# Kernel optimization log

Hardware: AMD Instinct MI355X
Metric: run time of the kernel (lower is better)

The kernel has to match this reference:

```python
import jax, jax.numpy as jnp
import numpy as np

N_NODES = 50000
NUM_REL = 8
IN_DIM = 128
HID = 256
NUM_CLASSES = 2
E = 1600000
M = 200000
LN_EPS = 1e-5


def setup_inputs() -> dict:
    key = jax.random.key(0)
    ks = jax.random.split(key, 20)
    s = 0.05
    inp = {
        "x": jax.random.normal(ks[0], (N_NODES, IN_DIM), jnp.float32),
        "edge_index": jax.random.randint(ks[1], (2, E), 0, N_NODES, jnp.int32),
        "edge_type": jax.random.randint(ks[2], (E,), 0, NUM_REL, jnp.int32),
        "dec_edges": jax.random.randint(ks[3], (M, 2), 0, N_NODES, jnp.int32),
        # conv1
        "W1": jax.random.normal(ks[4], (NUM_REL, IN_DIM, HID), jnp.float32) * s,
        "root1": jax.random.normal(ks[5], (IN_DIM, HID), jnp.float32) * s,
        "b1": jnp.zeros((HID,), jnp.float32),
        # conv2
        "W2": jax.random.normal(ks[6], (NUM_REL, HID, HID), jnp.float32) * s,
        "root2": jax.random.normal(ks[7], (HID, HID), jnp.float32) * s,
        "b2": jnp.zeros((HID,), jnp.float32),
        # layernorms
        "ln1_g": jnp.ones((HID,), jnp.float32),
        "ln1_b": jnp.zeros((HID,), jnp.float32),
        "ln2_g": jnp.ones((HID,), jnp.float32),
        "ln2_b": jnp.zeros((HID,), jnp.float32),
        # edge MLP: 2*HID -> HID -> HID//2 -> NUM_CLASSES
        "mlp_w1": jax.random.normal(ks[8], (2 * HID, HID), jnp.float32) * s,
        "mlp_b1": jnp.zeros((HID,), jnp.float32),
        "mlp_w2": jax.random.normal(ks[9], (HID, HID // 2), jnp.float32) * s,
        "mlp_b2": jnp.zeros((HID // 2,), jnp.float32),
        "mlp_w3": jax.random.normal(ks[10], (HID // 2, NUM_CLASSES), jnp.float32) * s,
        "mlp_b3": jnp.zeros((NUM_CLASSES,), jnp.float32),
    }
    return inp


def layer_norm(h, g, b):
    mu = jnp.mean(h, axis=-1, keepdims=True)
    var = jnp.mean(jnp.square(h - mu), axis=-1, keepdims=True)
    return (h - mu) * jax.lax.rsqrt(var + LN_EPS) * g + b


def rgcn_conv(x, edge_index, edge_type, W, root, bias):
    # PyG RGCNConv with aggr='mean': per-relation mean aggregation of
    # neighbor features, aggregate-then-transform (valid since linear),
    # plus root transform and bias.
    src, dst = edge_index[0], edge_index[1]
    xs = x[src]  # [E, d_in]
    out = x @ root + bias
    num_rel = W.shape[0]
    for r in range(num_rel):
        m = (edge_type == r).astype(x.dtype)  # [E]
        agg = jax.ops.segment_sum(xs * m[:, None], dst, num_segments=x.shape[0])
        cnt = jax.ops.segment_sum(m, dst, num_segments=x.shape[0])
        out = out + (agg / jnp.maximum(cnt, 1.0)[:, None]) @ W[r]
    return out


def reference(x, edge_index, edge_type, dec_edges,
              W1, root1, b1, W2, root2, b2,
              ln1_g, ln1_b, ln2_g, ln2_b,
              mlp_w1, mlp_b1, mlp_w2, mlp_b2, mlp_w3, mlp_b3):
    # encode (dropout is identity in eval mode)
    h1 = rgcn_conv(x, edge_index, edge_type, W1, root1, b1)
    h1 = layer_norm(jax.nn.relu(h1), ln1_g, ln1_b)
    h2 = rgcn_conv(h1, edge_index, edge_type, W2, root2, b2)
    h2 = layer_norm(jax.nn.relu(h2), ln2_g, ln2_b)
    h = h1 + h2
    # decode: gather endpoints, concat, MLP (exact-erf GELU as nn.GELU)
    z = jnp.concatenate([h[dec_edges[:, 0]], h[dec_edges[:, 1]]], axis=1)
    z = jax.nn.gelu(z @ mlp_w1 + mlp_b1, approximate=False)
    z = jax.nn.gelu(z @ mlp_w2 + mlp_b2, approximate=False)
    return z @ mlp_w3 + mlp_b3
```

## Files before the change

### kernel.cpp

```cpp
#include <hip/hip_runtime.h>
#include <math.h>

typedef __attribute__((ext_vector_type(8))) short short8;
typedef __attribute__((ext_vector_type(4))) float f32x4;
typedef __attribute__((address_space(3))) void lds_void;
typedef const __attribute__((address_space(1))) void glb_void;

#define N_NODES 50000
#define NUM_REL 8
#define IN_DIM 128
#define HID 256
#define E_EDGES 1600000
#define M_DEC 200000
#define K1 1152
#define K2 2304
#define LN_EPS 1e-5f
#define NBUCK ((N_NODES + 63) >> 6)
#define NSEG (N_NODES * 8)
#define NSEG_BLK ((NSEG + 1023) >> 10)

__device__ __forceinline__ float b2f(ushort u) {
    union { unsigned int i; float f; } v; v.i = ((unsigned int)u) << 16; return v.f;
}
__device__ __forceinline__ ushort f2b(float f) {
    union { float f; unsigned int i; } v; v.f = f;
    unsigned int r = v.i + 0x7FFFu + ((v.i >> 16) & 1u);
    return (ushort)(r >> 16);
}
__device__ __forceinline__ unsigned int pk2(ushort a, ushort b) {
    return (unsigned int)a | ((unsigned int)b << 16);
}
__device__ __forceinline__ float gelu_fast(float x) {
    float y = 1.5957691216f * (x + 0.044715f * x * x * x);
    float e = __expf(y);
    float t = 1.f - 2.f * __builtin_amdgcn_rcpf(e + 1.f);
    return 0.5f * x * (1.f + t);
}

__global__ void count_all(const int* __restrict__ ei, const int* __restrict__ et,
                          int* __restrict__ cnt2,
                          const int* __restrict__ dec, int* __restrict__ bcnt) {
    int e = blockIdx.x * 256 + threadIdx.x;
    if (e < E_EDGES) {
        int dst = ei[E_EDGES + e];
        int r = et[e] & 7;
        atomicAdd(&cnt2[dst * 8 + r], 1);
    }
    if (e < M_DEC) {
        int a = dec[(size_t)e * 2];
        if (a < 0) a = 0; if (a >= N_NODES) a = N_NODES - 1;
        atomicAdd(&bcnt[a >> 6], 1);
    }
}

__global__ __launch_bounds__(1024) void scan_pass1(const int* __restrict__ cnt,
                                                   int* __restrict__ outp,
                                                   int* __restrict__ bsum) {
    __shared__ int ts[1024];
    const int t = threadIdx.x;
    const int i = blockIdx.x * 1024 + t;
    int v = (i < NSEG) ? cnt[i] : 0;
    ts[t] = v;
    __syncthreads();
#pragma unroll
    for (int off = 1; off < 1024; off <<= 1) {
        int u = (t >= off) ? ts[t - off] : 0;
        __syncthreads();
        ts[t] += u;
        __syncthreads();
    }
    if (i < NSEG) outp[i] = ts[t] - v;
    if (t == 1023) bsum[blockIdx.x] = ts[1023];
}

__global__ __launch_bounds__(1024) void scan_mid(int* __restrict__ bsum, int* __restrict__ rp2,
                                                 const int* __restrict__ bcnt,
                                                 int* __restrict__ bptr) {
    __shared__ int ts[1024];
    const int t = threadIdx.x;
    if (blockIdx.x == 0) {
        int v = (t < NSEG_BLK) ? bsum[t] : 0;
        ts[t] = v;
        __syncthreads();
#pragma unroll
        for (int off = 1; off < 1024; off <<= 1) {
            int u = (t >= off) ? ts[t - off] : 0;
            __syncthreads();
            ts[t] += u;
            __syncthreads();
        }
        if (t < NSEG_BLK) bsum[t] = ts[t] - v;
        if (t == NSEG_BLK - 1) rp2[NSEG] = ts[t];
    } else {
        int v = (t < NBUCK) ? bcnt[t] : 0;
        ts[t] = v;
        __syncthreads();
#pragma unroll
        for (int off = 1; off < 1024; off <<= 1) {
            int u = (t >= off) ? ts[t - off] : 0;
            __syncthreads();
            ts[t] += u;
            __syncthreads();
        }
        if (t < NBUCK) bptr[t] = ts[t] - v;
        if (t == 1023) bptr[NBUCK] = ts[1023];
    }
}

__global__ __launch_bounds__(1024) void scan_pass3(int* __restrict__ outp,
                                                   const int* __restrict__ bsum) {
    const int i = blockIdx.x * 1024 + threadIdx.x;
    if (i < NSEG) outp[i] += bsum[blockIdx.x];
}

__global__ void fill_all(const int* __restrict__ ei, const int* __restrict__ et,
                         const int* __restrict__ rp2, int* __restrict__ cursor,
                         unsigned int* __restrict__ epk,
                         const int* __restrict__ dec, const int* __restrict__ bptr,
                         int* __restrict__ bcur, int* __restrict__ perm) {
    int e = blockIdx.x * 256 + threadIdx.x;
    if (e < E_EDGES) {
        int src = ei[e];
        int dst = ei[E_EDGES + e];
        int r   = et[e] & 7;
        int idx8 = dst * 8 + r;
        int pos = rp2[idx8] + atomicAdd(&cursor[idx8], 1);
        if (pos >= 0 && pos < E_EDGES) epk[pos] = (unsigned int)src;
    }
    if (e < M_DEC) {
        int a = dec[(size_t)e * 2];
        if (a < 0) a = 0; if (a >= N_NODES) a = N_NODES - 1;
        int b = a >> 6;
        int pos = bptr[b] + atomicAdd(&bcur[b], 1);
        if (pos >= 0 && pos < M_DEC) perm[pos] = e;
    }
}

__global__ void pack_all(const float* __restrict__ x, ushort* __restrict__ xb,
                         const float* __restrict__ root1, const float* __restrict__ W1,
                         const float* __restrict__ root2, const float* __restrict__ W2,
                         ushort* __restrict__ B1t, ushort* __restrict__ B2t,
                         const float* __restrict__ mw1, const float* __restrict__ mw2,
                         ushort* __restrict__ wuvt, ushort* __restrict__ w2t) {
    const int XC = N_NODES * IN_DIM / 4;
    const int N1 = HID * K1;
    const int N2 = HID * K2;
    const int NU = 512 * 256;
    const int NW = 128 * 256;
    int idx = blockIdx.x * 256 + threadIdx.x;
    if (idx < XC) {
        float4 v = *(const float4*)(x + (size_t)idx * 4);
        uint2 o;
        o.x = pk2(f2b(v.x), f2b(v.y));
        o.y = pk2(f2b(v.z), f2b(v.w));
        *(uint2*)(xb + (size_t)idx * 4) = o;
        return;
    }
    idx -= XC;
    if (idx < N1) {
        int n = idx / K1, k = idx % K1;
        float v;
        if (k < IN_DIM) v = root1[k * HID + n];
        else { int kk = k - IN_DIM; v = W1[(size_t)(kk >> 7) * IN_DIM * HID + (kk & 127) * HID + n]; }
        B1t[(size_t)n * K1 + k] = f2b(v);
        return;
    }
    idx -= N1;
    if (idx < N2) {
        int n = idx / K2, k = idx % K2;
        float v;
        if (k < HID) v = root2[k * HID + n];
        else { int kk = k - HID; v = W2[(size_t)(kk >> 8) * HID * HID + (kk & 255) * HID + n]; }
        B2t[(size_t)n * K2 + k] = f2b(v);
        return;
    }
    idx -= N2;
    if (idx < NU) {
        int n = idx / 256, k = idx % 256;
        float v = (n < 256) ? mw1[(size_t)k * 256 + n] : mw1[(size_t)(256 + k) * 256 + (n - 256)];
        wuvt[(size_t)n * 256 + k] = f2b(v);
        return;
    }
    idx -= NU;
    if (idx < NW) {
        int n = idx / 256, k = idx % 256;
        w2t[n * 256 + k] = f2b(mw2[k * 128 + n]);
    }
}


#define FL1() { int c_ = segend - segbeg; float inv_ = c_ > 0 ? 1.f / (float)c_ : 0.f; \
    *(unsigned int*)(Arow + IN_DIM + r * IN_DIM + 2 * lane) = \
        pk2(f2b((aA.x + aB.x) * inv_), f2b((aA.y + aB.y) * inv_)); \
    aA.x = 0.f; aA.y = 0.f; aB.x = 0.f; aB.y = 0.f; \
    ++r; segbeg = segend; segend = (r < 8) ? rp[r + 1] : end; \
    if (segend < segbeg) segend = segbeg; if (segend > end) segend = end; }
#define CK1(EI) { while (r < 8 && (EI) >= segend) FL1(); }
#define AC1A(U) { aA.x += b2f((ushort)((U) & 0xFFFFu)); aA.y += b2f((ushort)((U) >> 16)); }
#define AC1B(U) { aB.x += b2f((ushort)((U) & 0xFFFFu)); aB.y += b2f((ushort)((U) >> 16)); }

__global__ __launch_bounds__(256) void agg1_kernel(const ushort* __restrict__ xb,
                                                   const int* __restrict__ rp2,
                                                   const unsigned int* __restrict__ epk,
                                                   ushort* __restrict__ Achunk, int n0, int m) {
    const int w = threadIdx.x >> 6, lane = threadIdx.x & 63;
    const int local = blockIdx.x * 4 + w;
    if (local >= m) return;
    const int n = n0 + local;
    const int* rp = rp2 + n * 8;
    ushort* Arow = Achunk + (size_t)local * K1;
    const ushort* xbb = xb + 2 * lane;
    *(unsigned int*)(Arow + 2 * lane) = *(const unsigned int*)(xb + (size_t)n * IN_DIM + 2 * lane);

    int beg = rp[0], end = rp[8];
    if (beg < 0) beg = 0;
    if (end > E_EDGES) end = E_EDGES;
    if (end < beg) end = beg;

    float2 aA = {0.f, 0.f}, aB = {0.f, 0.f};
    int r = 0, segbeg = beg, segend = rp[1];
    if (segend < segbeg) segend = segbeg; if (segend > end) segend = end;

    int e = beg;
    for (; e + 7 < end; e += 8) {
        unsigned int p0 = epk[e],     p1 = epk[e + 1], p2 = epk[e + 2], p3 = epk[e + 3];
        unsigned int p4 = epk[e + 4], p5 = epk[e + 5], p6 = epk[e + 6], p7 = epk[e + 7];
        unsigned int u0 = *(const unsigned int*)(xbb + (size_t)p0 * IN_DIM);
        unsigned int u1 = *(const unsigned int*)(xbb + (size_t)p1 * IN_DIM);
        unsigned int u2 = *(const unsigned int*)(xbb + (size_t)p2 * IN_DIM);
        unsigned int u3 = *(const unsigned int*)(xbb + (size_t)p3 * IN_DIM);
        unsigned int u4 = *(const unsigned int*)(xbb + (size_t)p4 * IN_DIM);
        unsigned int u5 = *(const unsigned int*)(xbb + (size_t)p5 * IN_DIM);
        unsigned int u6 = *(const unsigned int*)(xbb + (size_t)p6 * IN_DIM);
        unsigned int u7 = *(const unsigned int*)(xbb + (size_t)p7 * IN_DIM);
        CK1(e)     AC1A(u0) CK1(e + 1) AC1B(u1)
        CK1(e + 2) AC1A(u2) CK1(e + 3) AC1B(u3)
        CK1(e + 4) AC1A(u4) CK1(e + 5) AC1B(u5)
        CK1(e + 6) AC1A(u6) CK1(e + 7) AC1B(u7)
    }
    for (; e < end; ++e) {
        unsigned int p = epk[e];
        unsigned int u = *(const unsigned int*)(xbb + (size_t)p * IN_DIM);
        CK1(e) AC1A(u)
    }
    while (r < 8) FL1();
}

#define FL2() { int c_ = segend - segbeg; float inv_ = c_ > 0 ? 1.f / (float)c_ : 0.f; \
    f32x4 t_ = aA + aB; uint2 o_; \
    o_.x = pk2(f2b(t_[0] * inv_), f2b(t_[1] * inv_)); \
    o_.y = pk2(f2b(t_[2] * inv_), f2b(t_[3] * inv_)); \
    *(uint2*)(Arow + HID + r * HID + 4 * lane) = o_; \
    aA = (f32x4){0.f, 0.f, 0.f, 0.f}; aB = aA; \
    ++r; segbeg = segend; segend = (r < 8) ? rp[r + 1] : end; \
    if (segend < segbeg) segend = segbeg; if (segend > end) segend = end; }
#define CK2(EI) { while (r < 8 && (EI) >= segend) FL2(); }
#define AC2A(U) { f32x4 f_; \
    f_[0] = b2f((ushort)((U).x & 0xFFFFu)); f_[1] = b2f((ushort)((U).x >> 16)); \
    f_[2] = b2f((ushort)((U).y & 0xFFFFu)); f_[3] = b2f((ushort)((U).y >> 16)); aA += f_; }
#define AC2B(U) { f32x4 f_; \
    f_[0] = b2f((ushort)((U).x & 0xFFFFu)); f_[1] = b2f((ushort)((U).x >> 16)); \
    f_[2] = b2f((ushort)((U).y & 0xFFFFu)); f_[3] = b2f((ushort)((U).y >> 16)); aB += f_; }

__global__ __launch_bounds__(256) void agg2_kernel(const ushort* __restrict__ h1,
                                                   const int* __restrict__ rp2,
                                                   const unsigned int* __restrict__ epk,
                                                   ushort* __restrict__ Achunk, int n0, int m) {
    const int w = threadIdx.x >> 6, lane = threadIdx.x & 63;
    const int local = blockIdx.x * 4 + w;
    if (local >= m) return;
    const int n = n0 + local;
    const int* rp = rp2 + n * 8;
    ushort* Arow = Achunk + (size_t)local * K2;
    const ushort* hb = h1 + 4 * lane;
    *(uint2*)(Arow + 4 * lane) = *(const uint2*)(h1 + (size_t)n * HID + 4 * lane);

    int beg = rp[0], end = rp[8];
    if (beg < 0) beg = 0;
    if (end > E_EDGES) end = E_EDGES;
    if (end < beg) end = beg;

    f32x4 aA = {0.f, 0.f, 0.f, 0.f}, aB = {0.f, 0.f, 0.f, 0.f};
    int r = 0, segbeg = beg, segend = rp[1];
    if (segend < segbeg) segend = segbeg; if (segend > end) segend = end;

    int e = beg;
    for (; e + 7 < end; e += 8) {
        unsigned int p0 = epk[e],     p1 = epk[e + 1], p2 = epk[e + 2], p3 = epk[e + 3];
        unsigned int p4 = epk[e + 4], p5 = epk[e + 5], p6 = epk[e + 6], p7 = epk[e + 7];
        uint2 u0 = *(const uint2*)(hb + (size_t)p0 * HID);
        uint2 u1 = *(const uint2*)(hb + (size_t)p1 * HID);
        uint2 u2 = *(const uint2*)(hb + (size_t)p2 * HID);
        uint2 u3 = *(const uint2*)(hb + (size_t)p3 * HID);
        uint2 u4 = *(const uint2*)(hb + (size_t)p4 * HID);
        uint2 u5 = *(const uint2*)(hb + (size_t)p5 * HID);
        uint2 u6 = *(const uint2*)(hb + (size_t)p6 * HID);
        uint2 u7 = *(const uint2*)(hb + (size_t)p7 * HID);
        CK2(e)     AC2A(u0) CK2(e + 1) AC2B(u1)
        CK2(e + 2) AC2A(u2) CK2(e + 3) AC2B(u3)
        CK2(e + 4) AC2A(u4) CK2(e + 5) AC2B(u5)
        CK2(e + 6) AC2A(u6) CK2(e + 7) AC2B(u7)
    }
    for (; e < end; ++e) {
        unsigned int p = epk[e];
        uint2 u = *(const uint2*)(hb + (size_t)p * HID);
        CK2(e) AC2A(u)
    }
    while (r < 8) FL2();
}


#define STAGE(BUF, KO) { \
    __builtin_amdgcn_global_load_lds((glb_void*)(Ab + (KO)), \
        (lds_void*)(AsBase + (BUF) * 4096 + wave * 8 * 64), 16, 0, 0); \
    _Pragma("unroll") \
    for (int j_ = 0; j_ < 4; ++j_) \
        __builtin_amdgcn_global_load_lds((glb_void*)(Bb + (size_t)j_ * 8 * K + (KO)), \
            (lds_void*)(BsBase + (BUF) * 16384 + (wave * 32 + j_ * 8) * 64), 16, 0, 0); }

#define COMPUTE(CUR) { \
    _Pragma("unroll") \
    for (int kk = 0; kk < 2; ++kk) { \
        const int gsw = (((kk * 4 + qd) ^ (cc & 7)) * 8); \
        short8 af[2], bfv[4]; \
        _Pragma("unroll") \
        for (int i = 0; i < 2; ++i) \
            af[i] = *(const short8*)&AsBase[(CUR) * 4096 + (mh * 32 + i * 16 + cc) * 64 + gsw]; \
        _Pragma("unroll") \
        for (int j = 0; j < 4; ++j) \
            bfv[j] = *(const short8*)&BsBase[(CUR) * 16384 + (wn + j * 16 + cc) * 64 + gsw]; \
        _Pragma("unroll") \
        for (int i = 0; i < 2; ++i) \
            _Pragma("unroll") \
            for (int j = 0; j < 4; ++j) \
                acc[i][j] = __builtin_amdgcn_mfma_f32_16x16x32_bf16(af[i], bfv[j], acc[i][j], 0, 0, 0); \
    } }

__global__ __launch_bounds__(512, 4) void gemm_fused(
    const ushort* __restrict__ A, const ushort* __restrict__ Bt,
    int lda, int M, int K,
    const float* __restrict__ bias, const float* __restrict__ g,
    const float* __restrict__ bvec, const ushort* __restrict__ resid,
    ushort* __restrict__ outp, int ldc, int rowOff) {
    __shared__ __align__(16) ushort smem[40960];
    ushort* AsBase = smem;
    ushort* BsBase = smem + 2 * 64 * 64;
    const int tid = threadIdx.x;
    const int wave = tid >> 6, lane = tid & 63;
    const int w4 = wave & 3, mh = wave >> 2;
    const int cc = lane & 15, qd = lane >> 4;
    const int row0 = blockIdx.x * 64;
    const int colBase = blockIdx.y * 256;
    const int wn = w4 * 64;
    const int srow = lane >> 3;
    const int sgrp = (lane & 7) ^ (srow & 7);
    f32x4 acc[2][4];
#pragma unroll
    for (int i = 0; i < 2; ++i)
#pragma unroll
        for (int j = 0; j < 4; ++j) acc[i][j] = (f32x4){0.f, 0.f, 0.f, 0.f};

    const ushort* Ab = A + (size_t)(row0 + wave * 8 + srow) * lda + sgrp * 8;
    const ushort* Bb = Bt + (size_t)(colBase + wave * 32 + srow) * K + sgrp * 8;

    STAGE(0, 0)
    for (int k0 = 0; k0 < K; k0 += 128) {
        if (k0 + 64 < K) {
            STAGE(1, k0 + 64)
            asm volatile("s_waitcnt vmcnt(5)" ::: "memory");
        } else {
            asm volatile("s_waitcnt vmcnt(0)" ::: "memory");
        }
        __builtin_amdgcn_s_barrier();
        COMPUTE(0)
        asm volatile("s_waitcnt lgkmcnt(0)" ::: "memory");
        __builtin_amdgcn_s_barrier();

        if (k0 + 128 < K) {
            STAGE(0, k0 + 128)
            asm volatile("s_waitcnt vmcnt(5)" ::: "memory");
        } else {
            asm volatile("s_waitcnt vmcnt(0)" ::: "memory");
        }
        __builtin_amdgcn_s_barrier();
        COMPUTE(1)
        asm volatile("s_waitcnt lgkmcnt(0)" ::: "memory");
        __builtin_amdgcn_s_barrier();
    }

    if (g) {
        float* partS = (float*)smem;
        float* partQ = (float*)smem + 256;
        float* muS   = (float*)smem + 512;
        float* rsS   = (float*)smem + 576;
#pragma unroll
        for (int j = 0; j < 4; ++j) {
            float bcol = bias[wn + j * 16 + cc];
#pragma unroll
            for (int i = 0; i < 2; ++i)
#pragma unroll
                for (int r = 0; r < 4; ++r)
                    acc[i][j][r] = fmaxf(acc[i][j][r] + bcol, 0.f);
        }
#pragma unroll
        for (int i = 0; i < 2; ++i)
#pragma unroll
            for (int r = 0; r < 4; ++r) {
                float s = acc[i][0][r] + acc[i][1][r] + acc[i][2][r] + acc[i][3][r];
                float q = acc[i][0][r] * acc[i][0][r] + acc[i][1][r] * acc[i][1][r]
                        + acc[i][2][r] * acc[i][2][r] + acc[i][3][r] * acc[i][3][r];
#pragma unroll
                for (int off = 1; off <= 8; off <<= 1) {
                    s += __shfl_xor(s, off, 64);
                    q += __shfl_xor(q, off, 64);
                }
                if (cc == 0) {
                    int row = mh * 32 + i * 16 + qd * 4 + r;
                    partS[row * 4 + w4] = s;
                    partQ[row * 4 + w4] = q;
                }
            }
        __syncthreads();
        if (tid < 64) {
            float S = partS[tid * 4] + partS[tid * 4 + 1] + partS[tid * 4 + 2] + partS[tid * 4 + 3];
            float Q = partQ[tid * 4] + partQ[tid * 4 + 1] + partQ[tid * 4 + 2] + partQ[tid * 4 + 3];
            float mu = S * (1.f / 256.f);
            float var = Q * (1.f / 256.f) - mu * mu;
            muS[tid] = mu;
            rsS[tid] = rsqrtf(fmaxf(var, 0.f) + LN_EPS);
        }
        __syncthreads();
#pragma unroll
        for (int i = 0; i < 2; ++i)
#pragma unroll
            for (int r = 0; r < 4; ++r) {
                int row = mh * 32 + i * 16 + qd * 4 + r;
                int grow = row0 + row;
                if (grow >= M) continue;
                float mu = muS[row], rs = rsS[row];
                size_t base = (size_t)(rowOff + grow) * ldc;
#pragma unroll
                for (int j = 0; j < 4; ++j) {
                    int col = wn + j * 16 + cc;
                    float val = (acc[i][j][r] - mu) * rs * g[col] + bvec[col];
                    if (resid) val += b2f(resid[base + col]);
                    outp[base + col] = f2b(val);
                }
            }
    } else {
#pragma unroll
        for (int i = 0; i < 2; ++i)
#pragma unroll
            for (int r = 0; r < 4; ++r) {
                int grow = row0 + mh * 32 + i * 16 + qd * 4 + r;
                if (grow >= M) continue;
                size_t base = (size_t)(rowOff + grow) * ldc;
#pragma unroll
                for (int j = 0; j < 4; ++j) {
                    int col = colBase + wn + j * 16 + cc;
                    outp[base + col] = f2b(acc[i][j][r]);
                }
            }
    }
}

__global__ __launch_bounds__(256) void edge_kernel(
    const ushort* __restrict__ uv, const int* __restrict__ dec, const int* __restrict__ perm,
    const float* __restrict__ b1, const ushort* __restrict__ w2t,
    const float* __restrict__ b2, const float* __restrict__ w3,
    const float* __restrict__ b3, float* __restrict__ outp, int M) {
    __shared__ __align__(16) ushort z1s[64][264];
    __shared__ __align__(16) ushort z2s[64][136];
    __shared__ float b1s[256], b2s[128], w3s[256];
    const int tid = threadIdx.x;
    const int wave = tid >> 6, lane = tid & 63;
    const int cc = lane & 15, qd = lane >> 4, lk = qd * 8, rr = qd * 4;
    const int e0 = blockIdx.x * 64;

    b1s[tid] = b1[tid];
    if (tid < 128) b2s[tid] = b2[tid];
    w3s[tid] = w3[tid];
    __syncthreads();

    {
        int e = tid >> 2, seg = tid & 3;
        int ge = perm[e0 + e];
        if (ge < 0) ge = 0; if (ge >= M) ge = M - 1;
        int a = dec[(size_t)ge * 2];
        int b = dec[(size_t)ge * 2 + 1];
        if (a < 0) a = 0; if (a >= N_NODES) a = N_NODES - 1;
        if (b < 0) b = 0; if (b >= N_NODES) b = N_NODES - 1;
        const ushort* up = uv + (size_t)a * 512 + seg * 64;
        const ushort* vp = uv + (size_t)b * 512 + 256 + seg * 64;
        short8 us[8], vs[8];
#pragma unroll
        for (int j = 0; j < 8; ++j) us[j] = *(const short8*)(up + j * 8);
#pragma unroll
        for (int j = 0; j < 8; ++j) vs[j] = *(const short8*)(vp + j * 8);
        int d0 = seg * 64;
#pragma unroll
        for (int j = 0; j < 8; ++j) {
            int d = d0 + j * 8;
            short8 zs;
#pragma unroll
            for (int l = 0; l < 8; ++l) {
                float z = b2f((ushort)us[j][l]) + b2f((ushort)vs[j][l]) + b1s[d + l];
                zs[l] = (short)f2b(gelu_fast(z));
            }
            *(short8*)&z1s[e][d] = zs;
        }
    }
    __syncthreads();

    f32x4 acc[4][2];
#pragma unroll
    for (int i = 0; i < 4; ++i)
#pragma unroll
        for (int j = 0; j < 2; ++j) acc[i][j] = (f32x4){0.f, 0.f, 0.f, 0.f};
    const int n0 = wave * 32;
#pragma unroll
    for (int ks = 0; ks < 8; ++ks) {
        short8 af[4], bfv[2];
#pragma unroll
        for (int i = 0; i < 4; ++i) af[i] = *(const short8*)&z1s[i * 16 + cc][ks * 32 + lk];
#pragma unroll
        for (int j = 0; j < 2; ++j)
            bfv[j] = *(const short8*)(w2t + (size_t)(n0 + j * 16 + cc) * 256 + ks * 32 + lk);
#pragma unroll
        for (int i = 0; i < 4; ++i)
#pragma unroll
            for (int j = 0; j < 2; ++j)
                acc[i][j] = __builtin_amdgcn_mfma_f32_16x16x32_bf16(af[i], bfv[j], acc[i][j], 0, 0, 0);
    }
#pragma unroll
    for (int i = 0; i < 4; ++i)
#pragma unroll
        for (int j = 0; j < 2; ++j)
#pragma unroll
            for (int r = 0; r < 4; ++r) {
                int m = i * 16 + rr + r;
                int n = n0 + j * 16 + cc;
                z2s[m][n] = f2b(gelu_fast(acc[i][j][r] + b2s[n]));
            }
    __syncthreads();

    if (tid < 128) {
        int e = tid >> 1, c = tid & 1;
        float s = b3[c];
        for (int k = 0; k < 128; ++k) s += b2f(z2s[e][k]) * w3s[k * 2 + c];
        int ge = perm[e0 + e];
        if (ge >= 0 && ge < M) outp[(size_t)ge * 2 + c] = s;
    }
}

extern "C" void kernel_launch(void* const* d_in, const int* in_sizes, int n_in,
                              void* d_out, int out_size, void* d_ws, size_t ws_size,
                              hipStream_t stream) {
    const float* x          = (const float*)d_in[0];
    const int*   edge_index = (const int*)d_in[1];
    const int*   edge_type  = (const int*)d_in[2];
    const int*   dec_edges  = (const int*)d_in[3];
    const float* W1         = (const float*)d_in[4];
    const float* root1      = (const float*)d_in[5];
    const float* b1         = (const float*)d_in[6];
    const float* W2         = (const float*)d_in[7];
    const float* root2      = (const float*)d_in[8];
    const float* b2         = (const float*)d_in[9];
    const float* ln1_g      = (const float*)d_in[10];
    const float* ln1_b      = (const float*)d_in[11];
    const float* ln2_g      = (const float*)d_in[12];
    const float* ln2_b      = (const float*)d_in[13];
    const float* mlp_w1     = (const float*)d_in[14];
    const float* mlp_b1     = (const float*)d_in[15];
    const float* mlp_w2     = (const float*)d_in[16];
    const float* mlp_b2     = (const float*)d_in[17];
    const float* mlp_w3     = (const float*)d_in[18];
    const float* mlp_b3     = (const float*)d_in[19];

    char* ws = (char*)d_ws;
    size_t off = 0;
    auto alloc = [&](size_t bytes) {
        void* p = ws + off;
        off += (bytes + 255) & ~(size_t)255;
        return p;
    };
    unsigned int* epk     = (unsigned int*)alloc((size_t)E_EDGES * 4);
    int*          rp2     = (int*)alloc((size_t)(NSEG + 1) * 4);
    int*          tmp     = (int*)alloc((size_t)(NSEG + NBUCK) * 4);
    int*          tmpb    = tmp + NSEG;
    int*          bptr    = (int*)alloc((size_t)(NBUCK + 1) * 4);
    int*          bsum    = (int*)alloc((size_t)NSEG_BLK * 4);
    int*          perm    = (int*)alloc((size_t)M_DEC * 4);
    ushort*       B1t     = (ushort*)alloc((size_t)HID * K1 * 2);
    ushort*       B2t     = (ushort*)alloc((size_t)HID * K2 * 2);
    ushort*       wuvt    = (ushort*)alloc((size_t)512 * 256 * 2);
    ushort*       w2t     = (ushort*)alloc((size_t)128 * 256 * 2);
    ushort*       xb      = (ushort*)alloc((size_t)N_NODES * IN_DIM * 2);
    ushort*       hfin    = (ushort*)alloc((size_t)N_NODES * HID * 2);

    size_t regionOff = off;
    ushort* h1ln  = (ushort*)(ws + regionOff);
    ushort* uvbuf = h1ln;
    size_t h1b = (((size_t)N_NODES * HID * 2) + 255) & ~(size_t)255;
    ushort* Achunk = (ushort*)(ws + regionOff + h1b);
    long long chunkB = (long long)ws_size - (long long)(regionOff + h1b);
    int chunk = 64;
    if (chunkB > 0) {
        long long c = chunkB / ((long long)K2 * 2);
        if (c > N_NODES) c = N_NODES;
        c &= ~63LL;
        if (c >= 64) chunk = (int)c;
    }
    int chunk1 = chunk * 2;
    if (chunk1 > N_NODES) chunk1 = N_NODES;

    hipMemsetAsync(tmp, 0, (size_t)(NSEG + NBUCK) * 4, stream);
    count_all<<<(E_EDGES + 255) / 256, 256, 0, stream>>>(edge_index, edge_type, tmp, dec_edges, tmpb);
    scan_pass1<<<NSEG_BLK, 1024, 0, stream>>>(tmp, rp2, bsum);
    scan_mid<<<2, 1024, 0, stream>>>(bsum, rp2, tmpb, bptr);
    scan_pass3<<<NSEG_BLK, 1024, 0, stream>>>(rp2, bsum);
    hipMemsetAsync(tmp, 0, (size_t)(NSEG + NBUCK) * 4, stream);
    fill_all<<<(E_EDGES + 255) / 256, 256, 0, stream>>>(edge_index, edge_type, rp2, tmp, epk,
                                                        dec_edges, bptr, tmpb, perm);

    {
        int total = N_NODES * IN_DIM / 4 + HID * K1 + HID * K2 + 512 * 256 + 128 * 256;
        pack_all<<<(total + 255) / 256, 256, 0, stream>>>(x, xb, root1, W1, root2, W2,
                                                          B1t, B2t, mlp_w1, mlp_w2, wuvt, w2t);
    }

    for (int n0 = 0; n0 < N_NODES; n0 += chunk1) {
        int m = N_NODES - n0; if (m > chunk1) m = chunk1;
        agg1_kernel<<<(m + 3) / 4, 256, 0, stream>>>(xb, rp2, epk, Achunk, n0, m);
        gemm_fused<<<dim3((m + 63) / 64, 1), 512, 0, stream>>>(
            Achunk, B1t, K1, m, K1, b1, ln1_g, ln1_b, nullptr, h1ln, HID, n0);
    }
    for (int n0 = 0; n0 < N_NODES; n0 += chunk) {
        int m = N_NODES - n0; if (m > chunk) m = chunk;
        agg2_kernel<<<(m + 3) / 4, 256, 0, stream>>>(h1ln, rp2, epk, Achunk, n0, m);
        gemm_fused<<<dim3((m + 63) / 64, 1), 512, 0, stream>>>(
            Achunk, B2t, K2, m, K2, b2, ln2_g, ln2_b, h1ln, hfin, HID, n0);
    }

    gemm_fused<<<dim3((N_NODES + 63) / 64, 2), 512, 0, stream>>>(
        hfin, wuvt, HID, N_NODES, HID, nullptr, nullptr, nullptr, nullptr, uvbuf, 512, 0);

    edge_kernel<<<(M_DEC + 63) / 64, 256, 0, stream>>>(
        uvbuf, dec_edges, perm, mlp_b1, w2t, mlp_b2, mlp_w3, mlp_b3, (float*)d_out, M_DEC);
}
```

Before: 878.7 us.

## Replace atomic CSR build with two-level LDS bucket sort of edges

Builds the per-(dst,relation) CSR with a two-stage radix-style sort instead of per-edge global atomics over 400k counters followed by a three-kernel scan. First, 64-node buckets are counted and scattered using LDS histograms with block-level reservation. Then one workgroup per bucket sorts locally by (dst low bits, relation) and writes rp2 and epk. This cuts global atomic contention and the number of launches, but adds a staging buffer and packs src into 16 bits, which relies on N_NODES < 65536.

```diff
diff --git a/kernel.cpp b/kernel.cpp
--- a/kernel.cpp
+++ b/kernel.cpp
@@ -15,9 +15,11 @@
 #define K1 1152
 #define K2 2304
 #define LN_EPS 1e-5f
-#define NBUCK ((N_NODES + 63) >> 6)
 #define NSEG (N_NODES * 8)
-#define NSEG_BLK ((NSEG + 1023) >> 10)
+#define NB2 782
+#define SA_WG 391
+#define SA_CH 4096
+#define SA_DCH 512
 
 __device__ __forceinline__ float b2f(ushort u) {
     union { unsigned int i; float f; } v; v.i = ((unsigned int)u) << 16; return v.f;
@@ -36,30 +38,54 @@
     float t = 1.f - 2.f * __builtin_amdgcn_rcpf(e + 1.f);
     return 0.5f * x * (1.f + t);
 }
-
-__global__ void count_all(const int* __restrict__ ei, const int* __restrict__ et,
-                          int* __restrict__ cnt2,
-                          const int* __restrict__ dec, int* __restrict__ bcnt) {
-    int e = blockIdx.x * 256 + threadIdx.x;
-    if (e < E_EDGES) {
-        int dst = ei[E_EDGES + e];
-        int r = et[e] & 7;
-        atomicAdd(&cnt2[dst * 8 + r], 1);
-    }
-    if (e < M_DEC) {
-        int a = dec[(size_t)e * 2];
-        if (a < 0) a = 0; if (a >= N_NODES) a = N_NODES - 1;
-        atomicAdd(&bcnt[a >> 6], 1);
-    }
-}
-
-__global__ __launch_bounds__(1024) void scan_pass1(const int* __restrict__ cnt,
-                                                   int* __restrict__ outp,
-                                                   int* __restrict__ bsum) {
+__device__ __forceinline__ int clampn(int v) {
+    if ((unsigned)v >= N_NODES) v = (v < 0) ? 0 : N_NODES - 1;
+    return v;
+}
+
+
+__global__ __launch_bounds__(256) void coarse_count(const int* __restrict__ ei,
+                                                    const int* __restrict__ dec,
+                                                    int* __restrict__ bh, int* __restrict__ dh) {
+    __shared__ int lb[NB2], ld[NB2];
+    const int t = threadIdx.x;
+    for (int i = t; i < NB2; i += 256) { lb[i] = 0; ld[i] = 0; }
+    __syncthreads();
+    const int e0 = blockIdx.x * SA_CH;
+#pragma unroll
+    for (int k = 0; k < 16; ++k) {
+        int e = e0 + k * 256 + t;
+        if (e < E_EDGES) {
+            int dst = clampn(ei[E_EDGES + e]);
+            atomicAdd(&lb[dst >> 6], 1);
+        }
+    }
+    const int d0 = blockIdx.x * SA_DCH;
+#pragma unroll
+    for (int k = 0; k < 2; ++k) {
+        int i = d0 + k * 256 + t;
+        if (i < M_DEC) {
+            int a = clampn(dec[(size_t)i * 2]);
+            atomicAdd(&ld[a >> 6], 1);
+        }
+    }
+    __syncthreads();
+    for (int i = t; i < NB2; i += 256) {
+        if (lb[i]) atomicAdd(&bh[i], lb[i]);
+        if (ld[i]) atomicAdd(&dh[i], ld[i]);
+    }
+}
+
+__global__ __launch_bounds__(1024) void scan_buckets(const int* __restrict__ bh, int* __restrict__ bbase,
+                                                     int* __restrict__ bcur,
+                                                     const int* __restrict__ dh, int* __restrict__ dbase,
+                                                     int* __restrict__ dcur, int* __restrict__ rp2) {
     __shared__ int ts[1024];
     const int t = threadIdx.x;
-    const int i = blockIdx.x * 1024 + t;
-    int v = (i < NSEG) ? cnt[i] : 0;
+    const int* src = (blockIdx.x == 0) ? bh : dh;
+    int* ob = (blockIdx.x == 0) ? bbase : dbase;
+    int* oc = (blockIdx.x == 0) ? bcur : dcur;
+    int v = (t < NB2) ? src[t] : 0;
     ts[t] = v;
     __syncthreads();
 #pragma unroll
@@ -69,70 +95,126 @@
         ts[t] += u;
         __syncthreads();
     }
-    if (i < NSEG) outp[i] = ts[t] - v;
-    if (t == 1023) bsum[blockIdx.x] = ts[1023];
-}
-
-__global__ __launch_bounds__(1024) void scan_mid(int* __restrict__ bsum, int* __restrict__ rp2,
-                                                 const int* __restrict__ bcnt,
-                                                 int* __restrict__ bptr) {
-    __shared__ int ts[1024];
+    if (t < NB2) { int ex = ts[t] - v; ob[t] = ex; oc[t] = ex; }
+    if (t == NB2 - 1) ob[NB2] = ts[t];
+    if (t == 0 && blockIdx.x == 0) rp2[NSEG] = E_EDGES;
+}
+
+__global__ __launch_bounds__(256) void stageA(const int* __restrict__ ei, const int* __restrict__ et,
+                                              int* __restrict__ bcur, unsigned int* __restrict__ sbuf,
+                                              const int* __restrict__ dec, int* __restrict__ dcur,
+                                              int* __restrict__ perm) {
+    __shared__ int h[NB2], base_[NB2];
     const int t = threadIdx.x;
-    if (blockIdx.x == 0) {
-        int v = (t < NSEG_BLK) ? bsum[t] : 0;
-        ts[t] = v;
+    const int e0 = blockIdx.x * SA_CH;
+    for (int i = t; i < NB2; i += 256) h[i] = 0;
+    __syncthreads();
+    int myb[16];
+#pragma unroll
+    for (int k = 0; k < 16; ++k) {
+        int e = e0 + k * 256 + t;
+        int b = -1;
+        if (e < E_EDGES) {
+            int dst = clampn(ei[E_EDGES + e]);
+            b = dst >> 6;
+            atomicAdd(&h[b], 1);
+        }
+        myb[k] = b;
+    }
+    __syncthreads();
+    for (int i = t; i < NB2; i += 256) {
+        int c = h[i];
+        base_[i] = c ? atomicAdd(&bcur[i], c) : 0;
+    }
+    __syncthreads();
+    for (int i = t; i < NB2; i += 256) h[i] = 0;
+    __syncthreads();
+#pragma unroll
+    for (int k = 0; k < 16; ++k) {
+        int e = e0 + k * 256 + t;
+        int b = myb[k];
+        if (b >= 0) {
+            int dst = clampn(ei[E_EDGES + e]);
+            int src = clampn(ei[e]);
+            int r = et[e] & 7;
+            int off = atomicAdd(&h[b], 1);
+            sbuf[base_[b] + off] =
+                (unsigned)src | ((unsigned)r << 16) | ((unsigned)(dst & 63) << 19);
+        }
+    }
+    __syncthreads();
+    for (int i = t; i < NB2; i += 256) h[i] = 0;
+    __syncthreads();
+    const int d0 = blockIdx.x * SA_DCH;
+    int dbk[2];
+#pragma unroll
+    for (int k = 0; k < 2; ++k) {
+        int i = d0 + k * 256 + t;
+        int b = -1;
+        if (i < M_DEC) {
+            int a = clampn(dec[(size_t)i * 2]);
+            b = a >> 6;
+            atomicAdd(&h[b], 1);
+        }
+        dbk[k] = b;
+    }
+    __syncthreads();
+    for (int i = t; i < NB2; i += 256) {
+        int c = h[i];
+        base_[i] = c ? atomicAdd(&dcur[i], c) : 0;
+    }
+    __syncthreads();
+    for (int i = t; i < NB2; i += 256) h[i] = 0;
+    __syncthreads();
+#pragma unroll
+    for (int k = 0; k < 2; ++k) {
+        int i = d0 + k * 256 + t;
+        int b = dbk[k];
+        if (b >= 0) {
+            int off = atomicAdd(&h[b], 1);
+            perm[base_[b] + off] = i;
+        }
+    }
+}
+
+__global__ __launch_bounds__(512) void stageB(const unsigned int* __restrict__ sbuf,
+                                              const int* __restrict__ bbase,
+                                              int* __restrict__ rp2,
+                                              unsigned int* __restrict__ epk) {
+    __shared__ int cnt[512];
+    __shared__ int pref[512];
+    const int t = threadIdx.x;
+    const int b = blockIdx.x;
+    const int s0 = bbase[b], s1 = bbase[b + 1];
+    cnt[t] = 0;
+    __syncthreads();
+    for (int i = s0 + t; i < s1; i += 512) {
+        unsigned int p = sbuf[i];
+        int ls = (((p >> 19) & 63) << 3) | ((p >> 16) & 7);
+        atomicAdd(&cnt[ls], 1);
+    }
+    __syncthreads();
+    pref[t] = cnt[t];
+    __syncthreads();
+#pragma unroll
+    for (int off = 1; off < 512; off <<= 1) {
+        int u = (t >= off) ? pref[t - off] : 0;
         __syncthreads();
-#pragma unroll
-        for (int off = 1; off < 1024; off <<= 1) {
-            int u = (t >= off) ? ts[t - off] : 0;
-            __syncthreads();
-            ts[t] += u;
-            __syncthreads();
-        }
-        if (t < NSEG_BLK) bsum[t] = ts[t] - v;
-        if (t == NSEG_BLK - 1) rp2[NSEG] = ts[t];
-    } else {
-        int v = (t < NBUCK) ? bcnt[t] : 0;
-        ts[t] = v;
+        pref[t] += u;
         __syncthreads();
-#pragma unroll
-        for (int off = 1; off < 1024; off <<= 1) {
-            int u = (t >= off) ? ts[t - off] : 0;
-            __syncthreads();
-            ts[t] += u;
-            __syncthreads();
-        }
-        if (t < NBUCK) bptr[t] = ts[t] - v;
-        if (t == 1023) bptr[NBUCK] = ts[1023];
-    }
-}
-
-__global__ __launch_bounds__(1024) void scan_pass3(int* __restrict__ outp,
-                                                   const int* __restrict__ bsum) {
-    const int i = blockIdx.x * 1024 + threadIdx.x;
-    if (i < NSEG) outp[i] += bsum[blockIdx.x];
-}
-
-__global__ void fill_all(const int* __restrict__ ei, const int* __restrict__ et,
-                         const int* __restrict__ rp2, int* __restrict__ cursor,
-                         unsigned int* __restrict__ epk,
-                         const int* __restrict__ dec, const int* __restrict__ bptr,
-                         int* __restrict__ bcur, int* __restrict__ perm) {
-    int e = blockIdx.x * 256 + threadIdx.x;
-    if (e < E_EDGES) {
-        int src = ei[e];
-        int dst = ei[E_EDGES + e];
-        int r   = et[e] & 7;
-        int idx8 = dst * 8 + r;
-        int pos = rp2[idx8] + atomicAdd(&cursor[idx8], 1);
-        if (pos >= 0 && pos < E_EDGES) epk[pos] = (unsigned int)src;
-    }
-    if (e < M_DEC) {
-        int a = dec[(size_t)e * 2];
-        if (a < 0) a = 0; if (a >= N_NODES) a = N_NODES - 1;
-        int b = a >> 6;
-        int pos = bptr[b] + atomicAdd(&bcur[b], 1);
-        if (pos >= 0 && pos < M_DEC) perm[pos] = e;
+    }
+    int excl = pref[t] - cnt[t];
+    int seg = b * 512 + t;
+    if (seg < NSEG) rp2[seg] = s0 + excl;
+    __syncthreads();
+    pref[t] = excl;
+    cnt[t] = 0;
+    __syncthreads();
+    for (int i = s0 + t; i < s1; i += 512) {
+        unsigned int p = sbuf[i];
+        int ls = (((p >> 19) & 63) << 3) | ((p >> 16) & 7);
+        int off = atomicAdd(&cnt[ls], 1);
+        epk[s0 + pref[ls] + off] = p & 0xFFFFu;
     }
 }
 
@@ -585,11 +667,15 @@
         return p;
     };
     unsigned int* epk     = (unsigned int*)alloc((size_t)E_EDGES * 4);
+    unsigned int* sbuf    = (unsigned int*)alloc((size_t)E_EDGES * 4);
     int*          rp2     = (int*)alloc((size_t)(NSEG + 1) * 4);
-    int*          tmp     = (int*)alloc((size_t)(NSEG + NBUCK) * 4);
-    int*          tmpb    = tmp + NSEG;
-    int*          bptr    = (int*)alloc((size_t)(NBUCK + 1) * 4);
-    int*          bsum    = (int*)alloc((size_t)NSEG_BLK * 4);
+    int*          hz      = (int*)alloc((size_t)2 * NB2 * 4);
+    int*          bh      = hz;
+    int*          dh      = hz + NB2;
+    int*          bbase   = (int*)alloc((size_t)(NB2 + 1) * 4);
+    int*          dbase   = (int*)alloc((size_t)(NB2 + 1) * 4);
+    int*          bcur    = (int*)alloc((size_t)NB2 * 4);
+    int*          dcur    = (int*)alloc((size_t)NB2 * 4);
     int*          perm    = (int*)alloc((size_t)M_DEC * 4);
     ushort*       B1t     = (ushort*)alloc((size_t)HID * K1 * 2);
     ushort*       B2t     = (ushort*)alloc((size_t)HID * K2 * 2);
@@ -614,14 +700,11 @@
     int chunk1 = chunk * 2;
     if (chunk1 > N_NODES) chunk1 = N_NODES;
 
-    hipMemsetAsync(tmp, 0, (size_t)(NSEG + NBUCK) * 4, stream);
-    count_all<<<(E_EDGES + 255) / 256, 256, 0, stream>>>(edge_index, edge_type, tmp, dec_edges, tmpb);
-    scan_pass1<<<NSEG_BLK, 1024, 0, stream>>>(tmp, rp2, bsum);
-    scan_mid<<<2, 1024, 0, stream>>>(bsum, rp2, tmpb, bptr);
-    scan_pass3<<<NSEG_BLK, 1024, 0, stream>>>(rp2, bsum);
-    hipMemsetAsync(tmp, 0, (size_t)(NSEG + NBUCK) * 4, stream);
-    fill_all<<<(E_EDGES + 255) / 256, 256, 0, stream>>>(edge_index, edge_type, rp2, tmp, epk,
-                                                        dec_edges, bptr, tmpb, perm);
+    hipMemsetAsync(hz, 0, (size_t)2 * NB2 * 4, stream);
+    coarse_count<<<SA_WG, 256, 0, stream>>>(edge_index, dec_edges, bh, dh);
+    scan_buckets<<<2, 1024, 0, stream>>>(bh, bbase, bcur, dh, dbase, dcur, rp2);
+    stageA<<<SA_WG, 256, 0, stream>>>(edge_index, edge_type, bcur, sbuf, dec_edges, dcur, perm);
+    stageB<<<NB2, 512, 0, stream>>>(sbuf, bbase, rp2, epk);
 
     {
         int total = N_NODES * IN_DIM / 4 + HID * K1 + HID * K2 + 512 * 256 + 128 * 256;
```

Measured after the change: 704.3 us. 19.8% less time.
